# Optimization experiments

Hardware: AMD Instinct MI355X
Metric: run time of the kernel (lower is better)

Reference implementation:

```python
import jax, jax.numpy as jnp
import numpy as np

B, S, D, H = 2, 2048, 1024, 16
DK = D // H  # 64


def setup_inputs() -> dict:
    key = jax.random.key(0)
    ks = jax.random.split(key, 5)
    query_input = jax.random.normal(ks[0], (B, S, D), dtype=jnp.float32)
    # additive mask: 1.0 where attention is disallowed (causal upper triangle)
    mask = jnp.triu(jnp.ones((S, S), dtype=jnp.float32), k=1)[None, None, :, :]
    scale = 1.0 / np.sqrt(D)
    wq = jax.random.normal(ks[1], (D, D), dtype=jnp.float32) * scale
    wk = jax.random.normal(ks[2], (D, D), dtype=jnp.float32) * scale
    wv = jax.random.normal(ks[3], (D, D), dtype=jnp.float32) * scale
    wo = jax.random.normal(ks[4], (D, D), dtype=jnp.float32) * scale
    return {"query_input": query_input, "mask": mask, "wq": wq, "wk": wk, "wv": wv, "wo": wo}


def _split_heads(x):
    # [B, S, D] -> [B, H, S, DK]
    b, s, _ = x.shape
    return x.reshape(b, s, H, DK).transpose(0, 2, 1, 3)


def reference(query_input, mask, wq, wk, wv, wo):
    # self-attention: key_input = value_input = query_input
    q = _split_heads(query_input @ wq)  # [B, H, S, DK]
    k = _split_heads(query_input @ wk)
    v = _split_heads(query_input @ wv)
    scores = jnp.einsum('bhqd,bhkd->bhqk', q, k) / jnp.sqrt(jnp.float32(DK))
    scores = scores + mask * (-1e9)
    attn = jax.nn.softmax(scores, axis=-1)
    out = jnp.einsum('bhqk,bhkd->bhqd', attn, v)  # [B, H, S, DK]
    out = out.transpose(0, 2, 1, 3).reshape(query_input.shape[0], -1, D)
    return out @ wo
```

## Files before the change

kernel.cpp:

```cpp
#include <hip/hip_runtime.h>

typedef __attribute__((ext_vector_type(8))) short bf16x8;
typedef __attribute__((ext_vector_type(4))) float f32x4;
typedef __attribute__((ext_vector_type(4))) unsigned short u16x4;

#define S_LEN 2048
#define D_DIM 1024
#define NHEAD 16
#define DK 64
#define BH 32
#define MROWS 4096

__device__ __forceinline__ unsigned short f2bf(float f) {
    unsigned int u = __float_as_uint(f);
    u += 0x7fffu + ((u >> 16) & 1u);
    return (unsigned short)(u >> 16);
}

__device__ __forceinline__ unsigned int pk_bf16(float a, float b) {
    unsigned int r;
    asm("v_cvt_pk_bf16_f32 %0, %1, %2" : "=v"(r) : "v"(a), "v"(b));
    return r;
}

__device__ __forceinline__ float fexp2(float x) {
    return __builtin_amdgcn_exp2f(x);
}

__device__ __forceinline__ void gload16(const void* g, void* l) {
    __builtin_amdgcn_global_load_lds(
        (const __attribute__((address_space(1))) void*)g,
        (__attribute__((address_space(3))) void*)l, 16, 0, 0);
}

__global__ __launch_bounds__(256) void cast_x_kernel(const float* __restrict__ X,
                                                     unsigned short* __restrict__ Xb) {
    int idx = blockIdx.x * 256 + threadIdx.x;
    float4 v = ((const float4*)X)[idx];
    u16x4 o;
    o.x = f2bf(v.x); o.y = f2bf(v.y); o.z = f2bf(v.z); o.w = f2bf(v.w);
    ((u16x4*)Xb)[idx] = o;
}

__global__ __launch_bounds__(256) void wtrans_kernel(const float* __restrict__ wq,
                                                     const float* __restrict__ wk,
                                                     const float* __restrict__ wv,
                                                     const float* __restrict__ wo,
                                                     unsigned short* __restrict__ Wt) {
    int z = blockIdx.z;
    const float* W = (z == 0) ? wq : (z == 1) ? wk : (z == 2) ? wv : wo;
    unsigned short* O = Wt + (size_t)z * D_DIM * D_DIM;
    __shared__ float t[32][33];
    int tx = threadIdx.x, ty = threadIdx.y;
    int bx = blockIdx.x * 32;
    int by = blockIdx.y * 32;
#pragma unroll
    for (int i = 0; i < 4; ++i)
        t[ty + i * 8][tx] = W[(size_t)(by + ty + i * 8) * D_DIM + bx + tx];
    __syncthreads();
#pragma unroll
    for (int i = 0; i < 4; ++i)
        O[(size_t)(bx + ty + i * 8) * D_DIM + by + tx] = f2bf(t[tx][ty + i * 8]);
}

__device__ __forceinline__ void gemm_mainloop(const unsigned short* __restrict__ A,
                                              const unsigned short* __restrict__ Bt,
                                              int K, int m0, int n0,
                                              unsigned short* As, unsigned short* Bs,
                                              f32x4 acc[4][4]) {
    const int tid = threadIdx.x;
    const int lane = tid & 63, wid = tid >> 6;
    const int wr = wid >> 1, wc = wid & 1;
    const int fr = lane & 15, fk = (lane >> 4) * 8;
    for (int k0 = 0; k0 < K; k0 += 32) {
        __syncthreads();
#pragma unroll
        for (int c = 0; c < 2; ++c) {
            int idx = c * 256 + tid;
            int row = idx >> 2;
            int col = (idx & 3) * 8;
            int base = (c * 256 + wid * 64) * 8;
            gload16(&A[(size_t)(m0 + row) * K + k0 + col], &As[base]);
            gload16(&Bt[(size_t)(n0 + row) * K + k0 + col], &Bs[base]);
        }
        __syncthreads();
        bf16x8 af[4], bfr[4];
#pragma unroll
        for (int i = 0; i < 4; ++i)
            af[i] = *(const bf16x8*)&As[(wr * 64 + i * 16 + fr) * 32 + fk];
#pragma unroll
        for (int j = 0; j < 4; ++j)
            bfr[j] = *(const bf16x8*)&Bs[(wc * 64 + j * 16 + fr) * 32 + fk];
#pragma unroll
        for (int i = 0; i < 4; ++i)
#pragma unroll
            for (int j = 0; j < 4; ++j)
                acc[i][j] = __builtin_amdgcn_mfma_f32_16x16x32_bf16(af[i], bfr[j], acc[i][j], 0, 0, 0);
    }
}

#define QSCALE 0.18033688011112042f
__global__ __launch_bounds__(256) void gemm_qkv_kernel(const unsigned short* __restrict__ Xb,
                                                       const unsigned short* __restrict__ Wt,
                                                       unsigned short* __restrict__ QKV) {
    __shared__ __align__(16) unsigned short As[128 * 32];
    __shared__ __align__(16) unsigned short Bs[128 * 32];
    const unsigned short* Bt = Wt + (size_t)blockIdx.z * D_DIM * D_DIM;
    unsigned short* Out = QKV + (size_t)blockIdx.z * MROWS * D_DIM;
    int m0 = blockIdx.y * 128, n0 = blockIdx.x * 128;
    f32x4 acc[4][4] = {};
    gemm_mainloop(Xb, Bt, D_DIM, m0, n0, As, Bs, acc);
    const float qs = (blockIdx.z == 0) ? QSCALE : 1.0f;
    const int lane = threadIdx.x & 63, wid = threadIdx.x >> 6;
    const int wr = wid >> 1, wc = wid & 1;
#pragma unroll
    for (int i = 0; i < 4; ++i)
#pragma unroll
        for (int j = 0; j < 4; ++j)
#pragma unroll
            for (int r = 0; r < 4; ++r) {
                int gm = m0 + wr * 64 + i * 16 + (lane >> 4) * 4 + r;
                int gn = n0 + wc * 64 + j * 16 + (lane & 15);
                Out[(size_t)gm * D_DIM + gn] = f2bf(acc[i][j][r] * qs);
            }
}

__global__ __launch_bounds__(256) void vtrans_kernel(const unsigned short* __restrict__ V,
                                                     unsigned short* __restrict__ Vt) {
    __shared__ unsigned short tile[64][65];
    int bh = blockIdx.y;
    int b = bh >> 4, h = bh & 15;
    int s0 = blockIdx.x * 64;
    int t = threadIdx.x;
#pragma unroll
    for (int i = 0; i < 16; ++i) {
        int idx = i * 256 + t;
        int row = idx >> 6, col = idx & 63;
        tile[row][col] = V[((size_t)(b * S_LEN) + s0 + row) * D_DIM + h * DK + col];
    }
    __syncthreads();
#pragma unroll
    for (int i = 0; i < 16; ++i) {
        int idx = i * 256 + t;
        int dr = idx >> 6, sc = idx & 63;
        Vt[((size_t)bh * DK + dr) * S_LEN + s0 + sc] = tile[sc][dr];
    }
}

__global__ __launch_bounds__(512, 4) void attn_kernel(const unsigned short* __restrict__ QKV,
                                                      const unsigned short* __restrict__ Vt,
                                                      unsigned short* __restrict__ AO) {
    const int bh = blockIdx.x;
    const int y = blockIdx.y;
    const int qi = (y < 8) ? (15 - y) : (y - 8);
    const int tid = threadIdx.x, lane = tid & 63, wid = tid >> 6;
    const int fr = lane & 15, fkg = lane >> 4, fk = fkg * 8;
    const unsigned short* Q = QKV;
    const unsigned short* Kd = QKV + (size_t)MROWS * D_DIM;

    __shared__ __align__(16) unsigned short Ks[2][128][64];
    __shared__ __align__(16) unsigned short Vs[2][64][128];
    __shared__ __align__(16) unsigned short Ps[8][16][64];

    const int b = bh >> 4, h = bh & 15;
    const int rsw  = fr & 7;
    const int off0 = (fkg ^ rsw) * 8;
    const int off1 = ((4 + fkg) ^ rsw) * 8;

    const int i0 = tid, i1 = 512 + tid;
    const int kr0 = i0 >> 3, kc0 = ((i0 & 7) ^ (kr0 & 7)) * 8;
    const int kr1 = i1 >> 3, kc1 = ((i1 & 7) ^ (kr1 & 7)) * 8;
    const int vr0 = i0 >> 4, vc0 = ((i0 & 15) ^ (vr0 & 15)) * 8;
    const int vr1 = i1 >> 4, vc1 = ((i1 & 15) ^ (vr1 & 15)) * 8;
    const int sb0 = (wid * 64) * 8;
    const int sb1 = (512 + wid * 64) * 8;

    const int q0 = qi * 128;
    const int qr = q0 + wid * 16;

    bf16x8 qf0 = *(const bf16x8*)&Q[((size_t)(b * S_LEN) + qr + fr) * D_DIM + h * DK + fk];
    bf16x8 qf1 = *(const bf16x8*)&Q[((size_t)(b * S_LEN) + qr + fr) * D_DIM + h * DK + 32 + fk];

    f32x4 o[4] = {};
    float m = -1e30f, l = 0.f;
    const int ntiles = qi + 1;

    const unsigned short* kb = Kd + (size_t)(b * S_LEN) * D_DIM + h * DK;
    const unsigned short* vb = Vt + (size_t)bh * DK * S_LEN;

    gload16(kb + (size_t)kr0 * D_DIM + kc0, &Ks[0][0][0] + sb0);
    gload16(kb + (size_t)kr1 * D_DIM + kc1, &Ks[0][0][0] + sb1);
    gload16(vb + (size_t)vr0 * S_LEN + vc0, &Vs[0][0][0] + sb0);
    gload16(vb + (size_t)vr1 * S_LEN + vc1, &Vs[0][0][0] + sb1);
    __syncthreads();

    for (int t = 0; t < ntiles; ++t) {
        const int buf = t & 1;
        if (t + 1 < ntiles) {
            const int kt = (t + 1) * 128;
            gload16(kb + (size_t)(kt + kr0) * D_DIM + kc0, &Ks[buf ^ 1][0][0] + sb0);
            gload16(kb + (size_t)(kt + kr1) * D_DIM + kc1, &Ks[buf ^ 1][0][0] + sb1);
            gload16(vb + (size_t)vr0 * S_LEN + kt + vc0, &Vs[buf ^ 1][0][0] + sb0);
            gload16(vb + (size_t)vr1 * S_LEN + kt + vc1, &Vs[buf ^ 1][0][0] + sb1);
        }

        f32x4 s4[8];
        __builtin_amdgcn_s_setprio(1);
#pragma unroll
        for (int nj = 0; nj < 8; ++nj) {
            const unsigned short* krow = &Ks[buf][nj * 16 + fr][0];
            bf16x8 kf0 = *(const bf16x8*)&krow[off0];
            bf16x8 kf1 = *(const bf16x8*)&krow[off1];
            f32x4 z = {};
            z = __builtin_amdgcn_mfma_f32_16x16x32_bf16(kf0, qf0, z, 0, 0, 0);
            z = __builtin_amdgcn_mfma_f32_16x16x32_bf16(kf1, qf1, z, 0, 0, 0);
            s4[nj] = z;
        }
        __builtin_amdgcn_s_setprio(0);

        if (t == ntiles - 1) {
            const int qoff = wid * 16 + fr;
#pragma unroll
            for (int nj = 0; nj < 8; ++nj)
#pragma unroll
                for (int r = 0; r < 4; ++r)
                    s4[nj][r] = (nj * 16 + fkg * 4 + r > qoff) ? -1e30f : s4[nj][r];
        }

        float mg[8];
#pragma unroll
        for (int nj = 0; nj < 8; ++nj)
            mg[nj] = fmaxf(fmaxf(s4[nj][0], s4[nj][1]), fmaxf(s4[nj][2], s4[nj][3]));
        float mt = fmaxf(fmaxf(fmaxf(mg[0], mg[1]), fmaxf(mg[2], mg[3])),
                         fmaxf(fmaxf(mg[4], mg[5]), fmaxf(mg[6], mg[7])));
        mt = fmaxf(mt, __shfl_xor(mt, 16, 64));
        mt = fmaxf(mt, __shfl_xor(mt, 32, 64));
        if (!__all(mt <= m + 8.0f)) {
            float mn = fmaxf(m, mt);
            float corr = fexp2(m - mn);
            m = mn;
            l *= corr;
            o[0] *= corr; o[1] *= corr; o[2] *= corr; o[3] *= corr;
        }
        float ps = 0.f;
        unsigned int pw[8][2];
#pragma unroll
        for (int nj = 0; nj < 8; ++nj) {
            float p0 = fexp2(s4[nj][0] - m);
            float p1 = fexp2(s4[nj][1] - m);
            float p2 = fexp2(s4[nj][2] - m);
            float p3 = fexp2(s4[nj][3] - m);
            ps += (p0 + p1) + (p2 + p3);
            pw[nj][0] = pk_bf16(p0, p1);
            pw[nj][1] = pk_bf16(p2, p3);
        }
        ps += __shfl_xor(ps, 16, 64);
        ps += __shfl_xor(ps, 32, 64);
        l += ps;

#pragma unroll
        for (int hf = 0; hf < 2; ++hf) {
#pragma unroll
            for (int nj = 0; nj < 4; ++nj) {
                int chunk = nj * 2 + (fkg >> 1);
                int el = (fkg & 1) * 4;
                *(uint2*)&Ps[wid][fr][((chunk ^ rsw) << 3) + el] =
                    make_uint2(pw[hf * 4 + nj][0], pw[hf * 4 + nj][1]);
            }
            bf16x8 pf0 = *(const bf16x8*)&Ps[wid][fr][off0];
            bf16x8 pf1 = *(const bf16x8*)&Ps[wid][fr][off1];
            __builtin_amdgcn_s_setprio(1);
#pragma unroll
            for (int j = 0; j < 4; ++j) {
                const unsigned short* vrow = &Vs[buf][j * 16 + fr][0];
                bf16x8 vf0 = *(const bf16x8*)&vrow[((hf * 8 + fkg) ^ fr) * 8];
                bf16x8 vf1 = *(const bf16x8*)&vrow[((hf * 8 + 4 + fkg) ^ fr) * 8];
                o[j] = __builtin_amdgcn_mfma_f32_16x16x32_bf16(vf0, pf0, o[j], 0, 0, 0);
                o[j] = __builtin_amdgcn_mfma_f32_16x16x32_bf16(vf1, pf1, o[j], 0, 0, 0);
            }
            __builtin_amdgcn_s_setprio(0);
        }

        __syncthreads();
    }

    float inv = 1.0f / l;
    size_t rowoff = ((size_t)(b * S_LEN) + qr + fr) * D_DIM + h * DK;
#pragma unroll
    for (int j = 0; j < 4; ++j) {
        u16x4 w;
        w.x = f2bf(o[j][0] * inv); w.y = f2bf(o[j][1] * inv);
        w.z = f2bf(o[j][2] * inv); w.w = f2bf(o[j][3] * inv);
        *(u16x4*)&AO[rowoff + j * 16 + fkg * 4] = w;
    }
}

__global__ __launch_bounds__(256) void gemm_out_kernel(const unsigned short* __restrict__ AO,
                                                       const unsigned short* __restrict__ Wot,
                                                       float* __restrict__ out) {
    __shared__ __align__(16) unsigned short As[128 * 32];
    __shared__ __align__(16) unsigned short Bs[128 * 32];
    int m0 = blockIdx.y * 128, n0 = blockIdx.x * 128;
    f32x4 acc[4][4] = {};
    gemm_mainloop(AO, Wot, D_DIM, m0, n0, As, Bs, acc);
    const int lane = threadIdx.x & 63, wid = threadIdx.x >> 6;
    const int wr = wid >> 1, wc = wid & 1;
#pragma unroll
    for (int i = 0; i < 4; ++i)
#pragma unroll
        for (int j = 0; j < 4; ++j)
#pragma unroll
            for (int r = 0; r < 4; ++r) {
                int gm = m0 + wr * 64 + i * 16 + (lane >> 4) * 4 + r;
                int gn = n0 + wc * 64 + j * 16 + (lane & 15);
                out[(size_t)gm * D_DIM + gn] = acc[i][j][r];
            }
}

extern "C" void kernel_launch(void* const* d_in, const int* in_sizes, int n_in,
                              void* d_out, int out_size, void* d_ws, size_t ws_size,
                              hipStream_t stream) {
    (void)in_sizes; (void)n_in; (void)out_size; (void)ws_size;
    const float* X  = (const float*)d_in[0];
    const float* wq = (const float*)d_in[2];
    const float* wk = (const float*)d_in[3];
    const float* wv = (const float*)d_in[4];
    const float* wo = (const float*)d_in[5];

    char* ws = (char*)d_ws;
    unsigned short* Xb  = (unsigned short*)(ws);
    unsigned short* Wt  = (unsigned short*)(ws + ((size_t)8  << 20));
    unsigned short* QKV = (unsigned short*)(ws + ((size_t)16 << 20));
    unsigned short* Vt  = (unsigned short*)(ws + ((size_t)40 << 20));
    unsigned short* AO  = (unsigned short*)(ws + ((size_t)48 << 20));
    float* out = (float*)d_out;

    cast_x_kernel<<<4096, 256, 0, stream>>>(X, Xb);
    wtrans_kernel<<<dim3(32, 32, 4), dim3(32, 8), 0, stream>>>(wq, wk, wv, wo, Wt);
    gemm_qkv_kernel<<<dim3(8, 32, 3), 256, 0, stream>>>(Xb, Wt, QKV);
    vtrans_kernel<<<dim3(32, 32), 256, 0, stream>>>(QKV + (size_t)2 * MROWS * D_DIM, Vt);
    attn_kernel<<<dim3(32, 16), 512, 0, stream>>>(QKV, Vt, AO);
    gemm_out_kernel<<<dim3(8, 32), 256, 0, stream>>>(AO, Wt + (size_t)3 * D_DIM * D_DIM, out);
}
```

Before: 115.0 us.

## Give each attention wave two query row groups and single-buffer V tiles

The attention kernel now runs 256 threads (4 waves) per block, and each wave handles 32 query rows as two 16-row groups. Each K/V fragment read from LDS therefore feeds twice as many MFMAs, which cuts LDS traffic per FLOP. V is now single-buffered: its next tile is loaded after the PV stage, with an extra barrier, which frees LDS. In exchange, register pressure is higher (two sets of accumulators and scores), there are fewer waves to hide latency, and the V load is no longer overlapped with compute.

After: 119.1 us. 1.03x slower.

```diff
diff --git a/kernel.cpp b/kernel.cpp
--- a/kernel.cpp
+++ b/kernel.cpp
@@ -147,7 +147,7 @@
     }
 }
 
-__global__ __launch_bounds__(512, 4) void attn_kernel(const unsigned short* __restrict__ QKV,
+__global__ __launch_bounds__(256, 2) void attn_kernel(const unsigned short* __restrict__ QKV,
                                                       const unsigned short* __restrict__ Vt,
                                                       unsigned short* __restrict__ AO) {
     const int bh = blockIdx.x;
@@ -159,139 +159,187 @@
     const unsigned short* Kd = QKV + (size_t)MROWS * D_DIM;
 
     __shared__ __align__(16) unsigned short Ks[2][128][64];
-    __shared__ __align__(16) unsigned short Vs[2][64][128];
-    __shared__ __align__(16) unsigned short Ps[8][16][64];
+    __shared__ __align__(16) unsigned short Vs[64][128];
+    __shared__ __align__(16) unsigned short Ps[4][2][16][64];
 
     const int b = bh >> 4, h = bh & 15;
     const int rsw  = fr & 7;
     const int off0 = (fkg ^ rsw) * 8;
     const int off1 = ((4 + fkg) ^ rsw) * 8;
 
-    const int i0 = tid, i1 = 512 + tid;
-    const int kr0 = i0 >> 3, kc0 = ((i0 & 7) ^ (kr0 & 7)) * 8;
-    const int kr1 = i1 >> 3, kc1 = ((i1 & 7) ^ (kr1 & 7)) * 8;
-    const int vr0 = i0 >> 4, vc0 = ((i0 & 15) ^ (vr0 & 15)) * 8;
-    const int vr1 = i1 >> 4, vc1 = ((i1 & 15) ^ (vr1 & 15)) * 8;
-    const int sb0 = (wid * 64) * 8;
-    const int sb1 = (512 + wid * 64) * 8;
-
     const int q0 = qi * 128;
-    const int qr = q0 + wid * 16;
-
-    bf16x8 qf0 = *(const bf16x8*)&Q[((size_t)(b * S_LEN) + qr + fr) * D_DIM + h * DK + fk];
-    bf16x8 qf1 = *(const bf16x8*)&Q[((size_t)(b * S_LEN) + qr + fr) * D_DIM + h * DK + 32 + fk];
-
-    f32x4 o[4] = {};
-    float m = -1e30f, l = 0.f;
+    const int qr = q0 + wid * 32;
     const int ntiles = qi + 1;
 
     const unsigned short* kb = Kd + (size_t)(b * S_LEN) * D_DIM + h * DK;
     const unsigned short* vb = Vt + (size_t)bh * DK * S_LEN;
 
-    gload16(kb + (size_t)kr0 * D_DIM + kc0, &Ks[0][0][0] + sb0);
-    gload16(kb + (size_t)kr1 * D_DIM + kc1, &Ks[0][0][0] + sb1);
-    gload16(vb + (size_t)vr0 * S_LEN + vc0, &Vs[0][0][0] + sb0);
-    gload16(vb + (size_t)vr1 * S_LEN + vc1, &Vs[0][0][0] + sb1);
+    const unsigned short* qbase = Q + ((size_t)(b * S_LEN) + qr + fr) * D_DIM + h * DK;
+    bf16x8 qf[2][2];
+    qf[0][0] = *(const bf16x8*)&qbase[fk];
+    qf[0][1] = *(const bf16x8*)&qbase[32 + fk];
+    qf[1][0] = *(const bf16x8*)&qbase[16 * D_DIM + fk];
+    qf[1][1] = *(const bf16x8*)&qbase[16 * D_DIM + 32 + fk];
+
+    f32x4 o[2][4] = {};
+    float m[2] = {-1e30f, -1e30f}, l[2] = {0.f, 0.f};
+
+#pragma unroll
+    for (int c = 0; c < 4; ++c) {
+        int i = c * 256 + tid;
+        int kr = i >> 3, kc = ((i & 7) ^ (kr & 7)) * 8;
+        int vr = i >> 4, vc = ((i & 15) ^ (vr & 15)) * 8;
+        int base = (c * 256 + wid * 64) * 8;
+        gload16(kb + (size_t)kr * D_DIM + kc, &Ks[0][0][0] + base);
+        gload16(vb + (size_t)vr * S_LEN + vc, &Vs[0][0] + base);
+    }
     __syncthreads();
 
     for (int t = 0; t < ntiles; ++t) {
         const int buf = t & 1;
         if (t + 1 < ntiles) {
             const int kt = (t + 1) * 128;
-            gload16(kb + (size_t)(kt + kr0) * D_DIM + kc0, &Ks[buf ^ 1][0][0] + sb0);
-            gload16(kb + (size_t)(kt + kr1) * D_DIM + kc1, &Ks[buf ^ 1][0][0] + sb1);
-            gload16(vb + (size_t)vr0 * S_LEN + kt + vc0, &Vs[buf ^ 1][0][0] + sb0);
-            gload16(vb + (size_t)vr1 * S_LEN + kt + vc1, &Vs[buf ^ 1][0][0] + sb1);
-        }
-
-        f32x4 s4[8];
+#pragma unroll
+            for (int c = 0; c < 4; ++c) {
+                int i = c * 256 + tid;
+                int kr = i >> 3, kc = ((i & 7) ^ (kr & 7)) * 8;
+                int base = (c * 256 + wid * 64) * 8;
+                gload16(kb + (size_t)(kt + kr) * D_DIM + kc, &Ks[buf ^ 1][0][0] + base);
+            }
+        }
+
+        f32x4 s4[2][8];
         __builtin_amdgcn_s_setprio(1);
 #pragma unroll
         for (int nj = 0; nj < 8; ++nj) {
             const unsigned short* krow = &Ks[buf][nj * 16 + fr][0];
             bf16x8 kf0 = *(const bf16x8*)&krow[off0];
             bf16x8 kf1 = *(const bf16x8*)&krow[off1];
-            f32x4 z = {};
-            z = __builtin_amdgcn_mfma_f32_16x16x32_bf16(kf0, qf0, z, 0, 0, 0);
-            z = __builtin_amdgcn_mfma_f32_16x16x32_bf16(kf1, qf1, z, 0, 0, 0);
-            s4[nj] = z;
+            f32x4 z0 = {}, z1 = {};
+            z0 = __builtin_amdgcn_mfma_f32_16x16x32_bf16(kf0, qf[0][0], z0, 0, 0, 0);
+            z0 = __builtin_amdgcn_mfma_f32_16x16x32_bf16(kf1, qf[0][1], z0, 0, 0, 0);
+            z1 = __builtin_amdgcn_mfma_f32_16x16x32_bf16(kf0, qf[1][0], z1, 0, 0, 0);
+            z1 = __builtin_amdgcn_mfma_f32_16x16x32_bf16(kf1, qf[1][1], z1, 0, 0, 0);
+            s4[0][nj] = z0;
+            s4[1][nj] = z1;
         }
         __builtin_amdgcn_s_setprio(0);
 
         if (t == ntiles - 1) {
-            const int qoff = wid * 16 + fr;
-#pragma unroll
-            for (int nj = 0; nj < 8; ++nj)
-#pragma unroll
-                for (int r = 0; r < 4; ++r)
-                    s4[nj][r] = (nj * 16 + fkg * 4 + r > qoff) ? -1e30f : s4[nj][r];
-        }
-
-        float mg[8];
-#pragma unroll
-        for (int nj = 0; nj < 8; ++nj)
-            mg[nj] = fmaxf(fmaxf(s4[nj][0], s4[nj][1]), fmaxf(s4[nj][2], s4[nj][3]));
-        float mt = fmaxf(fmaxf(fmaxf(mg[0], mg[1]), fmaxf(mg[2], mg[3])),
-                         fmaxf(fmaxf(mg[4], mg[5]), fmaxf(mg[6], mg[7])));
-        mt = fmaxf(mt, __shfl_xor(mt, 16, 64));
-        mt = fmaxf(mt, __shfl_xor(mt, 32, 64));
-        if (!__all(mt <= m + 8.0f)) {
-            float mn = fmaxf(m, mt);
-            float corr = fexp2(m - mn);
-            m = mn;
-            l *= corr;
-            o[0] *= corr; o[1] *= corr; o[2] *= corr; o[3] *= corr;
-        }
-        float ps = 0.f;
-        unsigned int pw[8][2];
-#pragma unroll
-        for (int nj = 0; nj < 8; ++nj) {
-            float p0 = fexp2(s4[nj][0] - m);
-            float p1 = fexp2(s4[nj][1] - m);
-            float p2 = fexp2(s4[nj][2] - m);
-            float p3 = fexp2(s4[nj][3] - m);
-            ps += (p0 + p1) + (p2 + p3);
-            pw[nj][0] = pk_bf16(p0, p1);
-            pw[nj][1] = pk_bf16(p2, p3);
-        }
-        ps += __shfl_xor(ps, 16, 64);
-        ps += __shfl_xor(ps, 32, 64);
-        l += ps;
+#pragma unroll
+            for (int g = 0; g < 2; ++g) {
+                const int qoff = wid * 32 + g * 16 + fr;
+#pragma unroll
+                for (int nj = 0; nj < 8; ++nj)
+#pragma unroll
+                    for (int r = 0; r < 4; ++r)
+                        s4[g][nj][r] = (nj * 16 + fkg * 4 + r > qoff) ? -1e30f : s4[g][nj][r];
+            }
+        }
+
+        float mt[2];
+#pragma unroll
+        for (int g = 0; g < 2; ++g) {
+            float mg0 = fmaxf(fmaxf(s4[g][0][0], s4[g][0][1]), fmaxf(s4[g][0][2], s4[g][0][3]));
+            float mg1 = fmaxf(fmaxf(s4[g][1][0], s4[g][1][1]), fmaxf(s4[g][1][2], s4[g][1][3]));
+            float mg2 = fmaxf(fmaxf(s4[g][2][0], s4[g][2][1]), fmaxf(s4[g][2][2], s4[g][2][3]));
+            float mg3 = fmaxf(fmaxf(s4[g][3][0], s4[g][3][1]), fmaxf(s4[g][3][2], s4[g][3][3]));
+            float mg4 = fmaxf(fmaxf(s4[g][4][0], s4[g][4][1]), fmaxf(s4[g][4][2], s4[g][4][3]));
+            float mg5 = fmaxf(fmaxf(s4[g][5][0], s4[g][5][1]), fmaxf(s4[g][5][2], s4[g][5][3]));
+            float mg6 = fmaxf(fmaxf(s4[g][6][0], s4[g][6][1]), fmaxf(s4[g][6][2], s4[g][6][3]));
+            float mg7 = fmaxf(fmaxf(s4[g][7][0], s4[g][7][1]), fmaxf(s4[g][7][2], s4[g][7][3]));
+            float v = fmaxf(fmaxf(fmaxf(mg0, mg1), fmaxf(mg2, mg3)),
+                            fmaxf(fmaxf(mg4, mg5), fmaxf(mg6, mg7)));
+            v = fmaxf(v, __shfl_xor(v, 16, 64));
+            v = fmaxf(v, __shfl_xor(v, 32, 64));
+            mt[g] = v;
+        }
+        bool ok = (mt[0] <= m[0] + 8.0f) && (mt[1] <= m[1] + 8.0f);
+        if (!__all(ok)) {
+#pragma unroll
+            for (int g = 0; g < 2; ++g) {
+                float mn = fmaxf(m[g], mt[g]);
+                float corr = fexp2(m[g] - mn);
+                m[g] = mn;
+                l[g] *= corr;
+                o[g][0] *= corr; o[g][1] *= corr; o[g][2] *= corr; o[g][3] *= corr;
+            }
+        }
+        unsigned int pw[2][8][2];
+#pragma unroll
+        for (int g = 0; g < 2; ++g) {
+            float ps = 0.f;
+#pragma unroll
+            for (int nj = 0; nj < 8; ++nj) {
+                float p0 = fexp2(s4[g][nj][0] - m[g]);
+                float p1 = fexp2(s4[g][nj][1] - m[g]);
+                float p2 = fexp2(s4[g][nj][2] - m[g]);
+                float p3 = fexp2(s4[g][nj][3] - m[g]);
+                ps += (p0 + p1) + (p2 + p3);
+                pw[g][nj][0] = pk_bf16(p0, p1);
+                pw[g][nj][1] = pk_bf16(p2, p3);
+            }
+            ps += __shfl_xor(ps, 16, 64);
+            ps += __shfl_xor(ps, 32, 64);
+            l[g] += ps;
+        }
+
+        __syncthreads();
 
 #pragma unroll
         for (int hf = 0; hf < 2; ++hf) {
 #pragma unroll
-            for (int nj = 0; nj < 4; ++nj) {
-                int chunk = nj * 2 + (fkg >> 1);
-                int el = (fkg & 1) * 4;
-                *(uint2*)&Ps[wid][fr][((chunk ^ rsw) << 3) + el] =
-                    make_uint2(pw[hf * 4 + nj][0], pw[hf * 4 + nj][1]);
-            }
-            bf16x8 pf0 = *(const bf16x8*)&Ps[wid][fr][off0];
-            bf16x8 pf1 = *(const bf16x8*)&Ps[wid][fr][off1];
+            for (int g = 0; g < 2; ++g)
+#pragma unroll
+                for (int nj = 0; nj < 4; ++nj) {
+                    int chunk = nj * 2 + (fkg >> 1);
+                    int el = (fkg & 1) * 4;
+                    *(uint2*)&Ps[wid][g][fr][((chunk ^ rsw) << 3) + el] =
+                        make_uint2(pw[g][hf * 4 + nj][0], pw[g][hf * 4 + nj][1]);
+                }
+            bf16x8 pf[2][2];
+            pf[0][0] = *(const bf16x8*)&Ps[wid][0][fr][off0];
+            pf[0][1] = *(const bf16x8*)&Ps[wid][0][fr][off1];
+            pf[1][0] = *(const bf16x8*)&Ps[wid][1][fr][off0];
+            pf[1][1] = *(const bf16x8*)&Ps[wid][1][fr][off1];
             __builtin_amdgcn_s_setprio(1);
 #pragma unroll
             for (int j = 0; j < 4; ++j) {
-                const unsigned short* vrow = &Vs[buf][j * 16 + fr][0];
+                const unsigned short* vrow = &Vs[j * 16 + fr][0];
                 bf16x8 vf0 = *(const bf16x8*)&vrow[((hf * 8 + fkg) ^ fr) * 8];
                 bf16x8 vf1 = *(const bf16x8*)&vrow[((hf * 8 + 4 + fkg) ^ fr) * 8];
-                o[j] = __builtin_amdgcn_mfma_f32_16x16x32_bf16(vf0, pf0, o[j], 0, 0, 0);
-                o[j] = __builtin_amdgcn_mfma_f32_16x16x32_bf16(vf1, pf1, o[j], 0, 0, 0);
+                o[0][j] = __builtin_amdgcn_mfma_f32_16x16x32_bf16(vf0, pf[0][0], o[0][j], 0, 0, 0);
+                o[0][j] = __builtin_amdgcn_mfma_f32_16x16x32_bf16(vf1, pf[0][1], o[0][j], 0, 0, 0);
+                o[1][j] = __builtin_amdgcn_mfma_f32_16x16x32_bf16(vf0, pf[1][0], o[1][j], 0, 0, 0);
+                o[1][j] = __builtin_amdgcn_mfma_f32_16x16x32_bf16(vf1, pf[1][1], o[1][j], 0, 0, 0);
             }
             __builtin_amdgcn_s_setprio(0);
         }
 
         __syncthreads();
-    }
-
-    float inv = 1.0f / l;
-    size_t rowoff = ((size_t)(b * S_LEN) + qr + fr) * D_DIM + h * DK;
-#pragma unroll
-    for (int j = 0; j < 4; ++j) {
-        u16x4 w;
-        w.x = f2bf(o[j][0] * inv); w.y = f2bf(o[j][1] * inv);
-        w.z = f2bf(o[j][2] * inv); w.w = f2bf(o[j][3] * inv);
-        *(u16x4*)&AO[rowoff + j * 16 + fkg * 4] = w;
+        if (t + 1 < ntiles) {
+            const int kt = (t + 1) * 128;
+#pragma unroll
+            for (int c = 0; c < 4; ++c) {
+                int i = c * 256 + tid;
+                int vr = i >> 4, vc = ((i & 15) ^ (vr & 15)) * 8;
+                int base = (c * 256 + wid * 64) * 8;
+                gload16(vb + (size_t)vr * S_LEN + kt + vc, &Vs[0][0] + base);
+            }
+        }
+    }
+
+#pragma unroll
+    for (int g = 0; g < 2; ++g) {
+        float inv = 1.0f / l[g];
+        size_t rowoff = ((size_t)(b * S_LEN) + qr + g * 16 + fr) * D_DIM + h * DK;
+#pragma unroll
+        for (int j = 0; j < 4; ++j) {
+            u16x4 w;
+            w.x = f2bf(o[g][j][0] * inv); w.y = f2bf(o[g][j][1] * inv);
+            w.z = f2bf(o[g][j][2] * inv); w.w = f2bf(o[g][j][3] * inv);
+            *(u16x4*)&AO[rowoff + j * 16 + fkg * 4] = w;
+        }
     }
 }
 
@@ -339,6 +387,6 @@
     wtrans_kernel<<<dim3(32, 32, 4), dim3(32, 8), 0, stream>>>(wq, wk, wv, wo, Wt);
     gemm_qkv_kernel<<<dim3(8, 32, 3), 256, 0, stream>>>(Xb, Wt, QKV);
     vtrans_kernel<<<dim3(32, 32), 256, 0, stream>>>(QKV + (size_t)2 * MROWS * D_DIM, Vt);
-    attn_kernel<<<dim3(32, 16), 512, 0, stream>>>(QKV, Vt, AO);
+    attn_kernel<<<dim3(32, 16), 256, 0, stream>>>(QKV, Vt, AO);
     gemm_out_kernel<<<dim3(8, 32), 256, 0, stream>>>(AO, Wt + (size_t)3 * D_DIM * D_DIM, out);
 }
```
